# Optimization experiments

Hardware: AMD Instinct MI355X
Metric: run time of the kernel (lower is better)

The kernel has to match this reference:

```python
import jax, jax.numpy as jnp
import numpy as np
import math

B, T, S = 8, 8, 64
L = T * S            # 512 tokens per modality
D = 1024             # bi_hidden_size
H = 16               # bi_num_attention_heads
DH = D // H          # 64 head size (queries)
DKV = D // 2         # 512 kv projection size
SCALE = 1.0 / math.sqrt(DH)


def setup_inputs() -> dict:
    key = jax.random.key(0)
    ks = jax.random.split(key, 24)
    inp = {
        "input_tensor1": jax.random.normal(ks[0], (B, T, S, D), jnp.float32),
        "attention_mask1": jnp.zeros((B, 1, 1, L), jnp.float32),
        "input_tensor2": jax.random.normal(ks[1], (B, T, S, D), jnp.float32),
        "attention_mask2": jnp.zeros((B, 1, 1, L), jnp.float32),
        "input_tensor3": jax.random.normal(ks[2], (B, T, S, D), jnp.float32),
        "attention_mask3": jnp.zeros((B, 1, 1, L), jnp.float32),
    }
    # Linear params, stored as [in, out]; y = x @ W + b
    kidx = 3
    for i in (1, 2, 3):
        inp[f"w_q{i}"] = jax.random.normal(ks[kidx], (D, D), jnp.float32) * 0.02; kidx += 1
        inp[f"b_q{i}"] = jnp.zeros((D,), jnp.float32)
        inp[f"w_k{i}"] = jax.random.normal(ks[kidx], (D, DKV), jnp.float32) * 0.02; kidx += 1
        inp[f"b_k{i}"] = jnp.zeros((DKV,), jnp.float32)
        inp[f"w_v{i}"] = jax.random.normal(ks[kidx], (D, DKV), jnp.float32) * 0.02; kidx += 1
        inp[f"b_v{i}"] = jnp.zeros((DKV,), jnp.float32)
    return inp


def _heads(x):
    # [B, L, H*dh] -> [B, H, L, dh]
    b, l, d = x.shape
    return x.reshape(b, l, H, d // H).transpose(0, 2, 1, 3)


def _branch(q, k_a, k_b, v_a, v_b, bias):
    # keys/values concatenated along the per-head feature dim (dim 3)
    k = jnp.concatenate([k_a, k_b], axis=-1)          # [B,H,L,dh]
    v = jnp.concatenate([v_a, v_b], axis=-1)          # [B,H,L,dh]
    scores = jnp.einsum('bhqd,bhkd->bhqk', q, k) * SCALE + bias
    probs = jax.nn.softmax(scores, axis=-1)           # [B,H,L,L]
    ctx = jnp.einsum('bhqk,bhkd->bhqd', probs, v)     # [B,H,L,dh]
    ctx = ctx.transpose(0, 2, 1, 3).reshape(q.shape[0], T, S, D)
    return ctx, probs


def reference(input_tensor1, attention_mask1, input_tensor2, attention_mask2,
              input_tensor3, attention_mask3,
              w_q1, b_q1, w_k1, b_k1, w_v1, b_v1,
              w_q2, b_q2, w_k2, b_k2, w_v2, b_v2,
              w_q3, b_q3, w_k3, b_k3, w_v3, b_v3):
    b = input_tensor1.shape[0]
    x1 = input_tensor1.reshape(b, L, -1)
    x2 = input_tensor2.reshape(b, L, -1)
    x3 = input_tensor3.reshape(b, L, -1)
    m1 = attention_mask1.reshape(b, 1, 1, L)
    m2 = attention_mask2.reshape(b, 1, 1, L)
    m3 = attention_mask3.reshape(b, 1, 1, L)

    q1 = _heads(x1 @ w_q1 + b_q1); k1 = _heads(x1 @ w_k1 + b_k1); v1 = _heads(x1 @ w_v1 + b_v1)
    q2 = _heads(x2 @ w_q2 + b_q2); k2 = _heads(x2 @ w_k2 + b_k2); v2 = _heads(x2 @ w_v2 + b_v2)
    q3 = _heads(x3 @ w_q3 + b_q3); k3 = _heads(x3 @ w_k3 + b_k3); v3 = _heads(x3 @ w_v3 + b_v3)

    # branch 1: Q from modality2, KV from 1+3, mask bias from masks 1&3
    c1, p1 = _branch(q2, k1, k3, v1, v3, m1 + m3)
    # branch 2: Q from modality1, KV from 2+3, no mask bias
    c2, p2 = _branch(q1, k2, k3, v2, v3, jnp.zeros((), jnp.float32))
    # branch 3: Q from modality3, KV from 1+2, mask bias from masks 1&2
    c3, p3 = _branch(q3, k1, k2, v1, v2, m1 + m2)

    return (c2, c1, c3, (p2, p1, p3))
```

## Files before the change

### kernel.cpp

```cpp
#include <hip/hip_runtime.h>
#include <hip/hip_bf16.h>

typedef __bf16 bf16x8 __attribute__((ext_vector_type(8)));
typedef float f32x4 __attribute__((ext_vector_type(4)));

#define ATT_SCALE 0.125f

static __device__ __forceinline__ unsigned short f2bf(float f){
  unsigned u = __float_as_uint(f);
  u += 0x7fffu + ((u >> 16) & 1u);
  return (unsigned short)(u >> 16);
}
static __device__ __forceinline__ bf16x8 ld_bf8(const unsigned short* p){
  uint4 u = *(const uint4*)p;
  return __builtin_bit_cast(bf16x8, u);
}
static __device__ __forceinline__ f32x4 mfma16(bf16x8 a, bf16x8 b, f32x4 c){
  return __builtin_amdgcn_mfma_f32_16x16x32_bf16(a, b, c, 0, 0, 0);
}
static __device__ __forceinline__ void gload16(const unsigned short* g, unsigned short* l){
  __builtin_amdgcn_global_load_lds(
      (const __attribute__((address_space(1))) unsigned*)g,
      (__attribute__((address_space(3))) unsigned*)l, 16, 0, 0);
}

struct CastArgs { const float* src[3]; unsigned short* dst[3]; };
__global__ __launch_bounds__(256) void cast_f32_bf16(CastArgs a){
  const float* in = a.src[blockIdx.y];
  unsigned short* out = a.dst[blockIdx.y];
  int i = blockIdx.x*256 + threadIdx.x;
  float4 f = ((const float4*)in)[i];
  ushort4 o = {f2bf(f.x), f2bf(f.y), f2bf(f.z), f2bf(f.w)};
  ((ushort4*)out)[i] = o;
}

struct WtArgs { const float* src[9]; unsigned short* dst[9]; int N[9]; };
__global__ void wtrans(WtArgs a){
  int z = blockIdx.z;
  int N = a.N[z];
  int n0 = blockIdx.x*32;
  if(n0 >= N) return;
  int k0 = blockIdx.y*32;
  const float* W = a.src[z];
  unsigned short* WT = a.dst[z];
  __shared__ float t[32][33];
  int tx = threadIdx.x, ty = threadIdx.y;
  #pragma unroll
  for(int r=0;r<4;++r){
    int row = ty + r*8;
    t[row][tx] = W[(size_t)(k0+row)*N + n0+tx];
  }
  __syncthreads();
  #pragma unroll
  for(int r=0;r<4;++r){
    int row = ty + r*8;
    WT[(size_t)(n0+row)*1024 + k0+tx] = f2bf(t[tx][row]);
  }
}

struct GemmArgs {
  const unsigned short* X[3]; const unsigned short* WT[3];
  const float* bq[3]; const float* bk[3]; const float* bv[3];
  unsigned short* C[3];
};
__global__ __launch_bounds__(256) void gemm_qkv(GemmArgs g){
  __shared__ unsigned short As[128*32];
  __shared__ unsigned short Bs[128*32];
  int z = blockIdx.z;
  const unsigned short* A  = g.X[z];
  const unsigned short* Bt = g.WT[z];
  unsigned short* C = g.C[z];
  int tid = threadIdx.x;
  int wave = tid>>6, lane = tid&63, l15 = lane&15, l4 = lane>>4;
  int m0 = blockIdx.y*128, n0 = blockIdx.x*128;
  int wr = wave>>1, wc = wave&1;
  f32x4 acc[4][4];
  #pragma unroll
  for(int i=0;i<4;++i)
    #pragma unroll
    for(int j=0;j<4;++j) acc[i][j] = (f32x4){0.f,0.f,0.f,0.f};

  int c0r = tid,      row0 = c0r>>2, col0 = (c0r&3)*8;
  int c1r = tid+256,  row1 = c1r>>2, col1 = (c1r&3)*8;
  const unsigned short* a0p = A  + (size_t)(m0+row0)*1024 + col0;
  const unsigned short* a1p = A  + (size_t)(m0+row1)*1024 + col1;
  const unsigned short* b0p = Bt + (size_t)(n0+row0)*1024 + col0;
  const unsigned short* b1p = Bt + (size_t)(n0+row1)*1024 + col1;

  for(int k0=0; k0<1024; k0+=32){
    gload16(a0p + k0, &As[c0r*8]);
    gload16(a1p + k0, &As[c1r*8]);
    gload16(b0p + k0, &Bs[c0r*8]);
    gload16(b1p + k0, &Bs[c1r*8]);
    __syncthreads();
    bf16x8 af[4], bfr[4];
    #pragma unroll
    for(int t=0;t<4;++t){
      af[t]  = ld_bf8(&As[(wr*64 + t*16 + l15)*32 + 8*l4]);
      bfr[t] = ld_bf8(&Bs[(wc*64 + t*16 + l15)*32 + 8*l4]);
    }
    #pragma unroll
    for(int mt=0;mt<4;++mt)
      #pragma unroll
      for(int nt=0;nt<4;++nt)
        acc[mt][nt] = mfma16(af[mt], bfr[nt], acc[mt][nt]);
    __syncthreads();
  }

  #pragma unroll
  for(int mt=0;mt<4;++mt){
    #pragma unroll
    for(int nt=0;nt<4;++nt){
      int col = n0 + wc*64 + nt*16 + l15;
      float bb;
      if(col < 1024)      bb = g.bq[z][col];
      else if(col < 1536) bb = g.bk[z][col-1024];
      else                bb = g.bv[z][col-1536];
      #pragma unroll
      for(int r=0;r<4;++r){
        int row = m0 + wr*64 + mt*16 + l4*4 + r;
        C[(size_t)row*2048 + col] = f2bf(acc[mt][nt][r] + bb);
      }
    }
  }
}

struct VtArgs { const unsigned short* in[3]; unsigned short* out[3]; };
__global__ __launch_bounds__(256) void vtrans(VtArgs a){
  int z = blockIdx.z;
  const unsigned short* in = a.in[z];
  unsigned short* out = a.out[z];
  __shared__ unsigned short T[64][72];
  int r0 = blockIdx.x*64, c0 = blockIdx.y*64;
  int tid = threadIdx.x;
  #pragma unroll
  for(int p=0;p<4;++p){
    int e = p*1024 + tid*4;
    int row = e>>6, col = e&63;
    *(ushort4*)&T[row][col] = *(const ushort4*)&in[(size_t)(r0+row)*2048 + c0+col];
  }
  __syncthreads();
  #pragma unroll
  for(int p=0;p<4;++p){
    int e = p*1024 + tid*4;
    int orow = e>>6, ocol = e&63;
    ushort4 v = {T[ocol][orow], T[ocol+1][orow], T[ocol+2][orow], T[ocol+3][orow]};
    *(ushort4*)&out[(size_t)(c0+orow)*4096 + r0+ocol] = v;
  }
}

struct AttnArgs {
  const unsigned short* Q[3];  const unsigned short* Ka[3]; const unsigned short* Kb[3];
  const unsigned short* VTa[3]; const unsigned short* VTb[3];
  const float* mA[3]; const float* mB[3];
  float* ctx[3]; float* probs[3];
};
__global__ __launch_bounds__(256,4) void attn(AttnArgs A){
  __shared__ unsigned short Pl[16*512];
  __shared__ float2 red[4][16];
  int wg = blockIdx.x;
  int id = (wg & 7)*1536 + (wg >> 3);
  int br = id >> 12;
  int rem = id & 4095;
  int bh = rem >> 5, qt = rem & 31;
  int b = bh >> 4, h = bh & 15;
  const unsigned short* Q   = A.Q[br];
  const unsigned short* Ka  = A.Ka[br];
  const unsigned short* Kb  = A.Kb[br];
  const unsigned short* VTa = A.VTa[br];
  const unsigned short* VTb = A.VTb[br];
  const float* mA = A.mA[br];
  const float* mB = A.mB[br];
  float* ctx   = A.ctx[br];
  float* probs = A.probs[br];

  int tid = threadIdx.x, wave = tid>>6, lane = tid&63, l15 = lane&15, l4 = lane>>4;
  int q0 = qt*16;
  int xr = l15 & 7;

  const unsigned short* qp = Q + (size_t)(b*512 + q0 + l15)*2048 + h*64 + 8*l4;
  bf16x8 a0 = ld_bf8(qp);
  bf16x8 a1 = ld_bf8(qp + 32);

  int kb0 = wave*128;
  const unsigned short* kap = Ka + (size_t)(b*512 + kb0 + l15)*2048 + h*32 + 8*l4;
  const unsigned short* kbp = Kb + (size_t)(b*512 + kb0 + l15)*2048 + h*32 + 8*l4;
  bf16x8 ka[8], kb[8];
  #pragma unroll
  for(int t=0;t<8;++t){
    ka[t] = ld_bf8(kap + (size_t)t*16*2048);
    kb[t] = ld_bf8(kbp + (size_t)t*16*2048);
  }

  f32x4 msk[8];
  #pragma unroll
  for(int t=0;t<8;++t){
    f32x4 v = (f32x4){0.f,0.f,0.f,0.f};
    int c = b*512 + kb0 + t*16 + l4*4;
    if(mA) v += *(const f32x4*)&mA[c];
    if(mB) v += *(const f32x4*)&mB[c];
    msk[t] = v;
  }

  int d0 = wave*16 + l15;
  const unsigned short* vb0 = (d0<32 ? VTa + (size_t)(h*32+d0)*4096 : VTb + (size_t)(h*32+d0-32)*4096) + b*512;
  bf16x8 vpre[8];
  #pragma unroll
  for(int kc=0;kc<8;++kc) vpre[kc] = ld_bf8(vb0 + kc*32 + 8*l4);

  f32x4 s[8];
  #pragma unroll
  for(int t=0;t<8;++t){
    f32x4 acc = (f32x4){0.f,0.f,0.f,0.f};
    acc = mfma16(ka[t], a0, acc);
    acc = mfma16(kb[t], a1, acc);
    s[t] = acc;
  }

  float m = -1e30f;
  #pragma unroll
  for(int t=0;t<8;++t){
    s[t] = s[t]*ATT_SCALE + msk[t];
    m = fmaxf(m, fmaxf(fmaxf(s[t][0], s[t][1]), fmaxf(s[t][2], s[t][3])));
  }
  m = fmaxf(m, __shfl_xor(m, 16));
  m = fmaxf(m, __shfl_xor(m, 32));
  float sum = 0.f;
  #pragma unroll
  for(int t=0;t<8;++t){
    #pragma unroll
    for(int r=0;r<4;++r){
      s[t][r] = __expf(s[t][r] - m);
      sum += s[t][r];
    }
  }
  sum += __shfl_xor(sum, 16);
  sum += __shfl_xor(sum, 32);
  if(l4 == 0) red[wave][l15] = make_float2(m, sum);
  __syncthreads();

  float2 pr0 = red[0][l15], pr1 = red[1][l15], pr2 = red[2][l15], pr3 = red[3][l15];
  float M = fmaxf(fmaxf(pr0.x, pr1.x), fmaxf(pr2.x, pr3.x));
  float T = pr0.y*__expf(pr0.x - M) + pr1.y*__expf(pr1.x - M)
          + pr2.y*__expf(pr2.x - M) + pr3.y*__expf(pr3.x - M);
  float scale = __expf(m - M) / T;

  #pragma unroll
  for(int t=0;t<8;++t) s[t] = s[t]*scale;

  #pragma unroll
  for(int t=0;t<8;++t){
    int u16 = wave*16 + t*2 + (l4>>1);
    ushort4 pb = {f2bf(s[t][0]), f2bf(s[t][1]), f2bf(s[t][2]), f2bf(s[t][3])};
    *(ushort4*)&Pl[l15*512 + ((u16 ^ xr) << 3) + (l4&1)*4] = pb;
  }
  __syncthreads();

  const unsigned short* prow = Pl + l15*512;
  f32x4 accE = (f32x4){0.f,0.f,0.f,0.f}, accO = (f32x4){0.f,0.f,0.f,0.f};
  #pragma unroll
  for(int kc=0;kc<16;++kc){
    int u = kc*4 + l4;
    bf16x8 a = ld_bf8(prow + ((u ^ xr) << 3));
    bf16x8 bb = (kc < 8) ? vpre[kc] : ld_bf8(vb0 + kc*32 + 8*l4);
    if(kc & 1) accO = mfma16(a, bb, accO);
    else       accE = mfma16(a, bb, accE);
  }
  f32x4 acc = accE + accO;
  #pragma unroll
  for(int r=0;r<4;++r){
    int row = q0 + l4*4 + r;
    ctx[((size_t)(b*512+row))*1024 + h*64 + d0] = acc[r];
  }

  float* po = probs + ((size_t)bh*512 + q0 + l15)*512 + kb0 + l4*4;
  #pragma unroll
  for(int t=0;t<8;++t)
    *(f32x4*)&po[t*16] = s[t];
}

extern "C" void kernel_launch(void* const* d_in, const int* in_sizes, int n_in,
                              void* d_out, int out_size, void* d_ws, size_t ws_size,
                              hipStream_t stream){
  const float* x[3]    = {(const float*)d_in[0], (const float*)d_in[2], (const float*)d_in[4]};
  const float* mask[3] = {(const float*)d_in[1], (const float*)d_in[3], (const float*)d_in[5]};
  const float *wq[3], *bq[3], *wk[3], *bk[3], *wv[3], *bv[3];
  for(int i=0;i<3;++i){
    wq[i]=(const float*)d_in[6+6*i];  bq[i]=(const float*)d_in[7+6*i];
    wk[i]=(const float*)d_in[8+6*i];  bk[i]=(const float*)d_in[9+6*i];
    wv[i]=(const float*)d_in[10+6*i]; bv[i]=(const float*)d_in[11+6*i];
  }

  unsigned short* ws = (unsigned short*)d_ws;
  unsigned short *Xb[3], *WT[3], *QKV[3], *VT[3];
  for(int i=0;i<3;++i){
    Xb[i]  = ws + (size_t)i*4194304;
    VT[i]  = Xb[i];
    WT[i]  = ws + 12582912 + (size_t)i*2097152;
    QKV[i] = ws + 18874368 + (size_t)i*8388608;
  }

  CastArgs ca;
  for(int i=0;i<3;++i){ ca.src[i]=x[i]; ca.dst[i]=Xb[i]; }
  cast_f32_bf16<<<dim3(4096,3), 256, 0, stream>>>(ca);

  WtArgs wa;
  for(int i=0;i<3;++i){
    wa.src[3*i+0]=wq[i]; wa.dst[3*i+0]=WT[i];           wa.N[3*i+0]=1024;
    wa.src[3*i+1]=wk[i]; wa.dst[3*i+1]=WT[i]+1048576;   wa.N[3*i+1]=512;
    wa.src[3*i+2]=wv[i]; wa.dst[3*i+2]=WT[i]+1572864;   wa.N[3*i+2]=512;
  }
  wtrans<<<dim3(32,32,9), dim3(32,8), 0, stream>>>(wa);

  GemmArgs ga;
  for(int i=0;i<3;++i){
    ga.X[i]=Xb[i]; ga.WT[i]=WT[i]; ga.bq[i]=bq[i]; ga.bk[i]=bk[i]; ga.bv[i]=bv[i]; ga.C[i]=QKV[i];
  }
  gemm_qkv<<<dim3(16,32,3), 256, 0, stream>>>(ga);

  VtArgs va;
  for(int i=0;i<3;++i){ va.in[i]=QKV[i]+1536; va.out[i]=VT[i]; }
  vtrans<<<dim3(64,8,3), 256, 0, stream>>>(va);

  float* out = (float*)d_out;
  float* ctx2 = out;
  float* ctx1 = out + 4194304;
  float* ctx3 = out + 8388608;
  float* p2   = out + 12582912;
  float* p1   = out + 46137344;
  float* p3   = out + 79691776;

  AttnArgs aa;
  aa.Q[0]=QKV[0]; aa.Ka[0]=QKV[1]+1024; aa.Kb[0]=QKV[2]+1024; aa.VTa[0]=VT[1]; aa.VTb[0]=VT[2];
  aa.mA[0]=nullptr; aa.mB[0]=nullptr; aa.ctx[0]=ctx2; aa.probs[0]=p2;
  aa.Q[1]=QKV[1]; aa.Ka[1]=QKV[0]+1024; aa.Kb[1]=QKV[2]+1024; aa.VTa[1]=VT[0]; aa.VTb[1]=VT[2];
  aa.mA[1]=mask[0]; aa.mB[1]=mask[2]; aa.ctx[1]=ctx1; aa.probs[1]=p1;
  aa.Q[2]=QKV[2]; aa.Ka[2]=QKV[0]+1024; aa.Kb[2]=QKV[1]+1024; aa.VTa[2]=VT[0]; aa.VTb[2]=VT[1];
  aa.mA[2]=mask[0]; aa.mB[2]=mask[1]; aa.ctx[2]=ctx3; aa.probs[2]=p3;
  attn<<<12288, 256, 0, stream>>>(aa);
}
```

Before: 367.6 us.

## Cut attention kernel register pressure and replace syncthreads with LDS-only barriers

Removes the min-blocks-per-CU launch bound, splits the K loads into two halves of four tiles so fewer K fragments are live at once, and prefetches only four V chunks instead of eight. The mask is added inline instead of being held in registers. __syncthreads is replaced by a barrier that waits only on LDS counters, so outstanding global loads can stay in flight. The LDS XOR swizzle is widened from l15&7 to l15 to reduce bank conflicts, and a sched_barrier keeps the probs stores after the ctx writes. Less V prefetch and the split K loads may expose more global-load latency.

```diff
diff --git a/kernel.cpp b/kernel.cpp
--- a/kernel.cpp
+++ b/kernel.cpp
@@ -22,6 +22,11 @@
   __builtin_amdgcn_global_load_lds(
       (const __attribute__((address_space(1))) unsigned*)g,
       (__attribute__((address_space(3))) unsigned*)l, 16, 0, 0);
+}
+static __device__ __forceinline__ void lgkm_bar(){
+  asm volatile("s_waitcnt lgkmcnt(0)" ::: "memory");
+  __builtin_amdgcn_s_barrier();
+  __builtin_amdgcn_sched_barrier(0);
 }
 
 struct CastArgs { const float* src[3]; unsigned short* dst[3]; };
@@ -155,7 +160,7 @@
   const float* mA[3]; const float* mB[3];
   float* ctx[3]; float* probs[3];
 };
-__global__ __launch_bounds__(256,4) void attn(AttnArgs A){
+__global__ __launch_bounds__(256) void attn(AttnArgs A){
   __shared__ unsigned short Pl[16*512];
   __shared__ float2 red[4][16];
   int wg = blockIdx.x;
@@ -176,51 +181,61 @@
 
   int tid = threadIdx.x, wave = tid>>6, lane = tid&63, l15 = lane&15, l4 = lane>>4;
   int q0 = qt*16;
-  int xr = l15 & 7;
+  int kb0 = wave*128;
 
   const unsigned short* qp = Q + (size_t)(b*512 + q0 + l15)*2048 + h*64 + 8*l4;
   bf16x8 a0 = ld_bf8(qp);
   bf16x8 a1 = ld_bf8(qp + 32);
 
-  int kb0 = wave*128;
   const unsigned short* kap = Ka + (size_t)(b*512 + kb0 + l15)*2048 + h*32 + 8*l4;
   const unsigned short* kbp = Kb + (size_t)(b*512 + kb0 + l15)*2048 + h*32 + 8*l4;
-  bf16x8 ka[8], kb[8];
-  #pragma unroll
-  for(int t=0;t<8;++t){
-    ka[t] = ld_bf8(kap + (size_t)t*16*2048);
-    kb[t] = ld_bf8(kbp + (size_t)t*16*2048);
-  }
-
-  f32x4 msk[8];
+
+  int d0 = wave*16 + l15;
+  const unsigned short* vb0 = (d0<32 ? VTa + (size_t)(h*32+d0)*4096 : VTb + (size_t)(h*32+d0-32)*4096) + b*512;
+  bf16x8 vpre[4];
+  #pragma unroll
+  for(int kc=0;kc<4;++kc) vpre[kc] = ld_bf8(vb0 + kc*32 + 8*l4);
+
+  f32x4 s[8];
+  {
+    bf16x8 k0[4], k1[4];
+    #pragma unroll
+    for(int t=0;t<4;++t){
+      k0[t] = ld_bf8(kap + (size_t)t*16*2048);
+      k1[t] = ld_bf8(kbp + (size_t)t*16*2048);
+    }
+    #pragma unroll
+    for(int t=0;t<4;++t){
+      f32x4 acc = (f32x4){0.f,0.f,0.f,0.f};
+      acc = mfma16(k0[t], a0, acc);
+      acc = mfma16(k1[t], a1, acc);
+      s[t] = acc;
+    }
+  }
+  {
+    bf16x8 k0[4], k1[4];
+    #pragma unroll
+    for(int t=0;t<4;++t){
+      k0[t] = ld_bf8(kap + (size_t)(t+4)*16*2048);
+      k1[t] = ld_bf8(kbp + (size_t)(t+4)*16*2048);
+    }
+    #pragma unroll
+    for(int t=0;t<4;++t){
+      f32x4 acc = (f32x4){0.f,0.f,0.f,0.f};
+      acc = mfma16(k0[t], a0, acc);
+      acc = mfma16(k1[t], a1, acc);
+      s[t+4] = acc;
+    }
+  }
+
+  float m = -1e30f;
   #pragma unroll
   for(int t=0;t<8;++t){
     f32x4 v = (f32x4){0.f,0.f,0.f,0.f};
     int c = b*512 + kb0 + t*16 + l4*4;
     if(mA) v += *(const f32x4*)&mA[c];
     if(mB) v += *(const f32x4*)&mB[c];
-    msk[t] = v;
-  }
-
-  int d0 = wave*16 + l15;
-  const unsigned short* vb0 = (d0<32 ? VTa + (size_t)(h*32+d0)*4096 : VTb + (size_t)(h*32+d0-32)*4096) + b*512;
-  bf16x8 vpre[8];
-  #pragma unroll
-  for(int kc=0;kc<8;++kc) vpre[kc] = ld_bf8(vb0 + kc*32 + 8*l4);
-
-  f32x4 s[8];
-  #pragma unroll
-  for(int t=0;t<8;++t){
-    f32x4 acc = (f32x4){0.f,0.f,0.f,0.f};
-    acc = mfma16(ka[t], a0, acc);
-    acc = mfma16(kb[t], a1, acc);
-    s[t] = acc;
-  }
-
-  float m = -1e30f;
-  #pragma unroll
-  for(int t=0;t<8;++t){
-    s[t] = s[t]*ATT_SCALE + msk[t];
+    s[t] = s[t]*ATT_SCALE + v;
     m = fmaxf(m, fmaxf(fmaxf(s[t][0], s[t][1]), fmaxf(s[t][2], s[t][3])));
   }
   m = fmaxf(m, __shfl_xor(m, 16));
@@ -237,7 +252,7 @@
   sum += __shfl_xor(sum, 16);
   sum += __shfl_xor(sum, 32);
   if(l4 == 0) red[wave][l15] = make_float2(m, sum);
-  __syncthreads();
+  lgkm_bar();
 
   float2 pr0 = red[0][l15], pr1 = red[1][l15], pr2 = red[2][l15], pr3 = red[3][l15];
   float M = fmaxf(fmaxf(pr0.x, pr1.x), fmaxf(pr2.x, pr3.x));
@@ -252,17 +267,17 @@
   for(int t=0;t<8;++t){
     int u16 = wave*16 + t*2 + (l4>>1);
     ushort4 pb = {f2bf(s[t][0]), f2bf(s[t][1]), f2bf(s[t][2]), f2bf(s[t][3])};
-    *(ushort4*)&Pl[l15*512 + ((u16 ^ xr) << 3) + (l4&1)*4] = pb;
-  }
-  __syncthreads();
+    *(ushort4*)&Pl[l15*512 + ((u16 ^ l15) << 3) + (l4&1)*4] = pb;
+  }
+  lgkm_bar();
 
   const unsigned short* prow = Pl + l15*512;
   f32x4 accE = (f32x4){0.f,0.f,0.f,0.f}, accO = (f32x4){0.f,0.f,0.f,0.f};
   #pragma unroll
   for(int kc=0;kc<16;++kc){
     int u = kc*4 + l4;
-    bf16x8 a = ld_bf8(prow + ((u ^ xr) << 3));
-    bf16x8 bb = (kc < 8) ? vpre[kc] : ld_bf8(vb0 + kc*32 + 8*l4);
+    bf16x8 a = ld_bf8(prow + ((u ^ l15) << 3));
+    bf16x8 bb = (kc < 4) ? vpre[kc] : ld_bf8(vb0 + kc*32 + 8*l4);
     if(kc & 1) accO = mfma16(a, bb, accO);
     else       accE = mfma16(a, bb, accE);
   }
@@ -273,6 +288,7 @@
     ctx[((size_t)(b*512+row))*1024 + h*64 + d0] = acc[r];
   }
 
+  __builtin_amdgcn_sched_barrier(0);
   float* po = probs + ((size_t)bh*512 + q0 + l15)*512 + kb0 + l4*4;
   #pragma unroll
   for(int t=0;t<8;++t)
```

Result: slower. 377.1 us (+2.6%).
